# Performance work log

Measured on AMD Instinct MI355X. Metric: run time of the kernel, lower is better.

The kernel has to match this reference:

```python
import jax, jax.numpy as jnp
import numpy as np
from jax import lax

N_PTS = 500000
CH = 64
GRID = 256
BN_EPS = 1e-5
A = -0.75  # torch bicubic coefficient


def setup_inputs() -> dict:
    key = jax.random.key(0)
    ks = jax.random.split(key, 10)
    coordinates = jax.random.uniform(ks[0], (N_PTS, 3), jnp.float32) * 2.0 - 1.0  # points in [-1,1]^3
    noise = jax.random.normal(ks[1], (3, N_PTS, 2), jnp.float32) * 0.01  # per-plane coord jitter (is_training)
    plane_x = jax.random.normal(ks[2], (1, CH, GRID, GRID), jnp.float32) * 0.001
    plane_y = jax.random.normal(ks[3], (1, CH, GRID, GRID), jnp.float32) * 0.001
    plane_z = jax.random.normal(ks[4], (1, CH, GRID, GRID), jnp.float32) * 0.001
    fan_in = CH * 9
    conv_w = jax.random.uniform(ks[5], (CH, CH, 3, 3), jnp.float32, -1.0, 1.0) / np.sqrt(fan_in)
    conv_b = jax.random.uniform(ks[6], (CH,), jnp.float32, -1.0, 1.0) / np.sqrt(fan_in)
    bn_gamma = jnp.ones((CH,), jnp.float32)
    bn_beta = jnp.zeros((CH,), jnp.float32)
    return {"coordinates": coordinates, "noise": noise, "plane_x": plane_x,
            "plane_y": plane_y, "plane_z": plane_z, "conv_w": conv_w,
            "conv_b": conv_b, "bn_gamma": bn_gamma, "bn_beta": bn_beta}


def res_block(p, conv_w, conv_b, gamma, beta):
    # conv3x3 stride2 pad1 -> BN (batch stats, training mode) -> relu, + avgpool3x3 s2 p1 (count_include_pad)
    y = lax.conv_general_dilated(p, conv_w, (2, 2), [(1, 1), (1, 1)],
                                 dimension_numbers=("NCHW", "OIHW", "NCHW"))
    y = y + conv_b[None, :, None, None]
    mu = jnp.mean(y, axis=(0, 2, 3), keepdims=True)
    var = jnp.var(y, axis=(0, 2, 3), keepdims=True)  # biased, as torch BN uses for normalization
    y = (y - mu) * lax.rsqrt(var + BN_EPS) * gamma[None, :, None, None] + beta[None, :, None, None]
    y = jax.nn.relu(y)
    pooled = lax.reduce_window(p, 0.0, lax.add, (1, 1, 3, 3), (1, 1, 2, 2),
                               [(0, 0), (0, 0), (1, 1), (1, 1)]) / 9.0
    return y + pooled


def cubic_weights(t):
    # torch cubic convolution weights, a=-0.75; t in [0,1). returns (4, M)
    t1 = t + 1.0
    w0 = ((A * t1 - 5 * A) * t1 + 8 * A) * t1 - 4 * A
    w1 = ((A + 2) * t - (A + 3)) * t * t + 1.0
    s = 1.0 - t
    w2 = ((A + 2) * s - (A + 3)) * s * s + 1.0
    w3 = 1.0 - w0 - w1 - w2
    return jnp.stack([w0, w1, w2, w3])


def sample_plane_bicubic(plane, grid):
    # plane: (C,H,W); grid: (M,2) with grid[:,0]->W axis, grid[:,1]->H axis (torch grid_sample layout)
    # bicubic, padding_mode='border', align_corners=True
    C, H, W = plane.shape
    gx = jnp.clip((grid[:, 0] + 1.0) * 0.5 * (W - 1), 0.0, W - 1.0)
    gy = jnp.clip((grid[:, 1] + 1.0) * 0.5 * (H - 1), 0.0, H - 1.0)
    x0f = jnp.floor(gx); y0f = jnp.floor(gy)
    tx = gx - x0f; ty = gy - y0f
    x0 = x0f.astype(jnp.int32); y0 = y0f.astype(jnp.int32)
    wx = cubic_weights(tx)  # (4,M)
    wy = cubic_weights(ty)  # (4,M)
    pl = jnp.transpose(plane, (1, 2, 0))  # (H,W,C)
    out = jnp.zeros((grid.shape[0], C), plane.dtype)
    for i in range(4):  # fixed 4x4 bicubic footprint
        yi = jnp.clip(y0 + (i - 1), 0, H - 1)
        for j in range(4):
            xi = jnp.clip(x0 + (j - 1), 0, W - 1)
            out = out + (wy[i] * wx[j])[:, None] * pl[yi, xi]
    return out  # (M,C)


def reference(coordinates, noise, plane_x, plane_y, plane_z, conv_w, conv_b, bn_gamma, bn_beta):
    bound = 1.0
    c = (coordinates + bound) / (2.0 * bound)  # (N,3) in [0,1] (fed to grid_sample as-is, faithful)
    px = res_block(plane_x, conv_w, conv_b, bn_gamma, bn_beta)[0]  # (C,128,128)
    py = res_block(plane_y, conv_w, conv_b, bn_gamma, bn_beta)[0]
    pz = res_block(plane_z, conv_w, conv_b, bn_gamma, bn_beta)[0]
    xy = sample_plane_bicubic(px, c[:, 0:2] + noise[0])
    yz = sample_plane_bicubic(py, c[:, 1:3] + noise[1])
    xz = sample_plane_bicubic(pz, c[:, 0:3:2] + noise[2])
    return xy + yz + xz  # (N,C)
```

## Files before the change

kernel.cpp:

```cpp
#include <hip/hip_runtime.h>
#include <hip/hip_fp16.h>

#define N_POINTS 500000
#define BN_EPS 1e-5f
#define A_COEF -0.75f

typedef __attribute__((ext_vector_type(8))) short short8;
typedef __attribute__((ext_vector_type(4))) float floatx4;
typedef unsigned short ushort_t;
typedef unsigned int uint_t;

#define WS_WBF_OFF    0
#define WS_CONV_OFF   18432
#define WS_SUM_OFF    (WS_CONV_OFF + 3145728)
#define WS_SUMSQ_OFF  (WS_SUM_OFF + 192)
#define WS_SCALE_OFF  (WS_SUMSQ_OFF + 192)
#define WS_SHIFT_OFF  (WS_SCALE_OFF + 192)
#define WS_PLANES_OFF (WS_SHIFT_OFF + 192)
#define WS_INBF_OFF   (WS_PLANES_OFF + 1572864)

__device__ __forceinline__ ushort_t f2bf(float f) {
  uint_t u = __float_as_uint(f);
  uint_t r = (u + 0x7fffu + ((u >> 16) & 1u)) >> 16;
  return (ushort_t)r;
}
__device__ __forceinline__ float bf2f(ushort_t u) {
  return __uint_as_float(((uint_t)u) << 16);
}

__global__ __launch_bounds__(256) void wprep_kernel(const float* __restrict__ w_in,
                                                    float* __restrict__ ws) {
  int i = blockIdx.x * 256 + threadIdx.x;
  if (i < 36864) {
    int ic = i & 63;
    int oc = (i >> 6) & 63;
    int kk = i >> 12;
    ((ushort_t*)(ws + WS_WBF_OFF))[i] = f2bf(w_in[(oc * 64 + ic) * 9 + kk]);
  }
  if (i < 384) ws[WS_SUM_OFF + i] = 0.0f;
}

__global__ __launch_bounds__(256) void transpose_kernel(const float* __restrict__ p0,
                                                        const float* __restrict__ p1,
                                                        const float* __restrict__ p2,
                                                        float* __restrict__ ws) {
  __shared__ float tile[64][65];
  const int xt = blockIdx.x, y = blockIdx.y, pl = blockIdx.z;
  const float* src = (pl == 0) ? p0 : ((pl == 1) ? p1 : p2);
  ushort_t* dst = (ushort_t*)(ws + WS_INBF_OFF) + pl * (256 * 256 * 64);
  const int t = threadIdx.x;
  const int x0 = xt * 64;
  for (int i = t; i < 4096; i += 256) {
    int c = i >> 6, x = i & 63;
    tile[x][c] = src[(c * 256 + y) * 256 + x0 + x];
  }
  __syncthreads();
  uint_t* du = (uint_t*)dst;
  for (int i = t; i < 2048; i += 256) {
    int x = i >> 5, cp = (i & 31) * 2;
    uint_t lo = f2bf(tile[x][cp]);
    uint_t hi = f2bf(tile[x][cp + 1]);
    du[((y * 256 + x0 + x) * 64 + cp) >> 1] = (hi << 16) | lo;
  }
}

__global__ __launch_bounds__(256) void conv_mfma_kernel(const float* __restrict__ ws_r,
                                                        float* __restrict__ ws) {
  const int xh = blockIdx.x, oy = blockIdx.y, pz = blockIdx.z;
  const int t = threadIdx.x;
  const int wv = t >> 6, lane = t & 63;
  const int mn = lane & 15;
  const int kg = lane >> 4;
  const int x0w = xh * 64 + wv * 16;

  const ushort_t* inb = (const ushort_t*)(ws_r + WS_INBF_OFF) + pz * (256 * 256 * 64);
  const ushort_t* wbf = (const ushort_t*)(ws_r + WS_WBF_OFF);

  floatx4 acc[4] = {{0.f,0.f,0.f,0.f},{0.f,0.f,0.f,0.f},{0.f,0.f,0.f,0.f},{0.f,0.f,0.f,0.f}};

  for (int ky = 0; ky < 3; ky++) {
    int y = 2 * oy - 1 + ky;
    if (y < 0) continue;
    const ushort_t* rowp = inb + y * (256 * 64);
    for (int kx = 0; kx < 3; kx++) {
      int xm = 2 * (x0w + mn) - 1 + kx;
      bool vx = xm >= 0;
      int xc = vx ? xm : 0;
      const ushort_t* abase = rowp + xc * 64 + kg * 8;
      const ushort_t* wbase = wbf + ((ky * 3 + kx) * 64 + mn) * 64 + kg * 8;
#pragma unroll
      for (int kc = 0; kc < 2; kc++) {
        union { int4 i4; short8 s8; } au;
        au.i4 = *reinterpret_cast<const int4*>(abase + kc * 32);
        if (!vx) au.i4 = make_int4(0, 0, 0, 0);
#pragma unroll
        for (int nt = 0; nt < 4; nt++) {
          union { int4 i4; short8 s8; } bu;
          bu.i4 = *reinterpret_cast<const int4*>(wbase + nt * 1024 + kc * 32);
          acc[nt] = __builtin_amdgcn_mfma_f32_16x16x32_bf16(au.s8, bu.s8, acc[nt], 0, 0, 0);
        }
      }
    }
  }
  float* cout = ws + WS_CONV_OFF + ((pz * 128 + oy) * 128 + x0w) * 64;
#pragma unroll
  for (int nt = 0; nt < 4; nt++) {
#pragma unroll
    for (int r = 0; r < 4; r++) {
      cout[(kg * 4 + r) * 64 + nt * 16 + mn] = acc[nt][r];
    }
  }
}

__global__ __launch_bounds__(256) void stats_kernel(float* __restrict__ ws) {
  const int b = blockIdx.x;
  const int plane = b >> 6, chunk = b & 63;
  const int t = threadIdx.x;
  const int c = t & 63, g = t >> 6;
  const float* base = ws + WS_CONV_OFF + plane * (16384 * 64);
  float s = 0.0f, s2 = 0.0f;
  const int row0 = chunk * 256 + g * 64;
  for (int i = 0; i < 64; i++) {
    float v = base[(row0 + i) * 64 + c];
    s += v;
    s2 = fmaf(v, v, s2);
  }
  __shared__ float rs[256], rs2[256];
  rs[t] = s; rs2[t] = s2;
  __syncthreads();
  if (t < 64) {
    s = rs[t] + rs[t + 64] + rs[t + 128] + rs[t + 192];
    s2 = rs2[t] + rs2[t + 64] + rs2[t + 128] + rs2[t + 192];
    atomicAdd(&ws[WS_SUM_OFF + plane * 64 + c], s);
    atomicAdd(&ws[WS_SUMSQ_OFF + plane * 64 + c], s2);
  }
}

__global__ void finalize_kernel(const float* __restrict__ gamma,
                                const float* __restrict__ beta,
                                float* __restrict__ ws) {
  int i = threadIdx.x;
  if (i < 192) {
    int c = i & 63;
    float mu = ws[WS_SUM_OFF + i] * (1.0f / 16384.0f);
    float var = ws[WS_SUMSQ_OFF + i] * (1.0f / 16384.0f) - mu * mu;
    var = fmaxf(var, 0.0f);
    float rstd = 1.0f / sqrtf(var + BN_EPS);
    float sc = gamma[c] * rstd;
    ws[WS_SCALE_OFF + i] = sc;
    ws[WS_SHIFT_OFF + i] = beta[c] - mu * sc;
  }
}

__global__ __launch_bounds__(256) void apply_kernel(float* __restrict__ ws,
                                                    __half* __restrict__ planes) {
  int idx = blockIdx.x * 256 + threadIdx.x;
  int g = idx & 7;
  int p = (idx >> 3) & 16383;
  int pl = idx >> 17;
  int oy = p >> 7, ox = p & 127;
  int cb = g * 8;

  const float* conv = ws + WS_CONV_OFF;
  float4 a0 = *reinterpret_cast<const float4*>(conv + (size_t)idx * 8);
  float4 a1 = *reinterpret_cast<const float4*>(conv + (size_t)idx * 8 + 4);

  float sc[8], sh[8];
#pragma unroll
  for (int k = 0; k < 8; k++) {
    sc[k] = ws[WS_SCALE_OFF + pl * 64 + cb + k];
    sh[k] = ws[WS_SHIFT_OFF + pl * 64 + cb + k];
  }

  const ushort_t* inb = (const ushort_t*)(ws + WS_INBF_OFF) + pl * (256 * 256 * 64);
  float ps[8];
#pragma unroll
  for (int k = 0; k < 8; k++) ps[k] = 0.0f;
#pragma unroll
  for (int r = 0; r < 3; r++) {
    int yy = 2 * oy - 1 + r;
    if (yy < 0) continue;
#pragma unroll
    for (int s = 0; s < 3; s++) {
      int xx = 2 * ox - 1 + s;
      if (xx < 0) continue;
      union { int4 i4; ushort_t u[8]; } ub;
      ub.i4 = *reinterpret_cast<const int4*>(inb + (yy * 256 + xx) * 64 + cb);
#pragma unroll
      for (int k = 0; k < 8; k++) ps[k] += bf2f(ub.u[k]);
    }
  }

  float v[8] = {a0.x, a0.y, a0.z, a0.w, a1.x, a1.y, a1.z, a1.w};
  union { int4 i4; __half h[8]; } ob;
#pragma unroll
  for (int k = 0; k < 8; k++) {
    float r = fmaxf(fmaf(v[k], sc[k], sh[k]), 0.0f) + ps[k] * (1.0f / 9.0f);
    ob.h[k] = __float2half(r);
  }
  *reinterpret_cast<int4*>(planes + (size_t)idx * 8) = ob.i4;
}

__device__ __forceinline__ void cubic_w(float t, float w[4]) {
  float t1 = t + 1.0f;
  w[0] = ((A_COEF * t1 - 5.0f * A_COEF) * t1 + 8.0f * A_COEF) * t1 - 4.0f * A_COEF;
  w[1] = ((A_COEF + 2.0f) * t - (A_COEF + 3.0f)) * t * t + 1.0f;
  float s = 1.0f - t;
  w[2] = ((A_COEF + 2.0f) * s - (A_COEF + 3.0f)) * s * s + 1.0f;
  w[3] = 1.0f - w[0] - w[1] - w[2];
}

__global__ __launch_bounds__(256) void sample_kernel(const float* __restrict__ coords,
                                                     const float* __restrict__ noise,
                                                     const __half* __restrict__ planes,
                                                     float* __restrict__ out) {
  const int t = threadIdx.x;
  const int wv = t >> 6, lane = t & 63;
  const int g = lane >> 3, l = lane & 7;
  const int n = blockIdx.x * 32 + wv * 8 + g;

  const float c0 = (coords[n * 3 + 0] + 1.0f) * 0.5f;
  const float c1 = (coords[n * 3 + 1] + 1.0f) * 0.5f;
  const float c2 = (coords[n * 3 + 2] + 1.0f) * 0.5f;

  float acc[8];
#pragma unroll
  for (int e = 0; e < 8; e++) acc[e] = 0.0f;

#pragma unroll
  for (int p = 0; p < 3; p++) {
    float u = (p == 1) ? c1 : c0;
    float v = (p == 0) ? c1 : c2;
    u += noise[(p * N_POINTS + n) * 2 + 0];
    v += noise[(p * N_POINTS + n) * 2 + 1];
    float gx = fminf(fmaxf(fmaf(u, 63.5f, 63.5f), 0.0f), 127.0f);
    float gy = fminf(fmaxf(fmaf(v, 63.5f, 63.5f), 0.0f), 127.0f);
    float x0f = floorf(gx), y0f = floorf(gy);
    float tx = gx - x0f, ty = gy - y0f;
    int ix = (int)x0f, iy = (int)y0f;
    float wx[4], wy[4];
    cubic_w(tx, wx);
    cubic_w(ty, wy);
    const __half* pb = planes + p * (128 * 128 * 64) + l * 8;
#pragma unroll
    for (int i = 0; i < 4; i++) {
      int yc = min(max(iy - 1 + i, 0), 127);
      const __half* rp = pb + yc * (128 * 64);
#pragma unroll
      for (int j = 0; j < 4; j++) {
        int xc = min(max(ix - 1 + j, 0), 127);
        union { int4 i4; __half2 h2[4]; } ub;
        ub.i4 = *reinterpret_cast<const int4*>(rp + xc * 64);
        float w = wy[i] * wx[j];
#pragma unroll
        for (int q = 0; q < 4; q++) {
          float2 f = __half22float2(ub.h2[q]);
          acc[2 * q]     = fmaf(f.x, w, acc[2 * q]);
          acc[2 * q + 1] = fmaf(f.y, w, acc[2 * q + 1]);
        }
      }
    }
  }
  float4* op = reinterpret_cast<float4*>(out + (size_t)n * 64 + l * 8);
  op[0] = make_float4(acc[0], acc[1], acc[2], acc[3]);
  op[1] = make_float4(acc[4], acc[5], acc[6], acc[7]);
}

extern "C" void kernel_launch(void* const* d_in, const int* in_sizes, int n_in,
                              void* d_out, int out_size, void* d_ws, size_t ws_size,
                              hipStream_t stream) {
  const float* coords = (const float*)d_in[0];
  const float* noise  = (const float*)d_in[1];
  const float* px     = (const float*)d_in[2];
  const float* py     = (const float*)d_in[3];
  const float* pz     = (const float*)d_in[4];
  const float* conv_w = (const float*)d_in[5];
  const float* gamma  = (const float*)d_in[7];
  const float* beta   = (const float*)d_in[8];
  float* out = (float*)d_out;
  float* ws = (float*)d_ws;
  __half* planes = (__half*)(ws + WS_PLANES_OFF);

  wprep_kernel<<<144, 256, 0, stream>>>(conv_w, ws);
  transpose_kernel<<<dim3(4, 256, 3), 256, 0, stream>>>(px, py, pz, ws);
  conv_mfma_kernel<<<dim3(2, 128, 3), 256, 0, stream>>>(ws, ws);
  stats_kernel<<<192, 256, 0, stream>>>(ws);
  finalize_kernel<<<1, 256, 0, stream>>>(gamma, beta, ws);
  apply_kernel<<<1536, 256, 0, stream>>>(ws, planes);
  sample_kernel<<<15625, 256, 0, stream>>>(coords, noise, planes, out);
}
```

Baseline: 366.4 us.

## Bin points spatially with a counting sort to localize plane gathers

Adds histogram, scan and scatter kernels that counting-sort the points into a 16x16x16 grid of cells. Each point is written as a packed record holding its three jittered plane coordinates and its original index. The sample kernel then walks the points in cell order, so neighbouring threads gather from nearby plane texels, which should improve L2 reuse of the fp16 planes. The cost is three extra passes over coords and noise, global atomics, and output rows now written in scattered order. The records reuse the bf16 input staging buffer once the conv stage is finished with it.

```diff
diff --git a/kernel.cpp b/kernel.cpp
--- a/kernel.cpp
+++ b/kernel.cpp
@@ -18,6 +18,8 @@
 #define WS_SHIFT_OFF  (WS_SCALE_OFF + 192)
 #define WS_PLANES_OFF (WS_SHIFT_OFF + 192)
 #define WS_INBF_OFF   (WS_PLANES_OFF + 1572864)
+#define WS_REC_OFF    WS_INBF_OFF
+#define WS_BIN_OFF    (WS_INBF_OFF + 6291456)
 
 __device__ __forceinline__ ushort_t f2bf(float f) {
   uint_t u = __float_as_uint(f);
@@ -26,6 +28,12 @@
 }
 __device__ __forceinline__ float bf2f(ushort_t u) {
   return __uint_as_float(((uint_t)u) << 16);
+}
+__device__ __forceinline__ int cell_of(float c0, float c1, float c2) {
+  int q0 = min(15, max(0, (int)(c0 * 16.0f)));
+  int q1 = min(15, max(0, (int)(c1 * 16.0f)));
+  int q2 = min(15, max(0, (int)(c2 * 16.0f)));
+  return (q0 << 8) | (q1 << 4) | q2;
 }
 
 __global__ __launch_bounds__(256) void wprep_kernel(const float* __restrict__ w_in,
@@ -38,6 +46,60 @@
     ((ushort_t*)(ws + WS_WBF_OFF))[i] = f2bf(w_in[(oc * 64 + ic) * 9 + kk]);
   }
   if (i < 384) ws[WS_SUM_OFF + i] = 0.0f;
+  if (i < 8192) ((int*)(ws + WS_BIN_OFF))[i] = 0;
+}
+
+__global__ __launch_bounds__(256) void hist_kernel(const float* __restrict__ coords,
+                                                   float* __restrict__ ws) {
+  int n = blockIdx.x * 256 + threadIdx.x;
+  if (n >= N_POINTS) return;
+  float c0 = (coords[n * 3 + 0] + 1.0f) * 0.5f;
+  float c1 = (coords[n * 3 + 1] + 1.0f) * 0.5f;
+  float c2 = (coords[n * 3 + 2] + 1.0f) * 0.5f;
+  atomicAdd(&((int*)(ws + WS_BIN_OFF))[cell_of(c0, c1, c2)], 1);
+}
+
+__global__ __launch_bounds__(256) void scan_kernel(float* __restrict__ ws) {
+  __shared__ int sums[256];
+  int* hist = (int*)(ws + WS_BIN_OFF);
+  int* offs = hist + 4096;
+  int t = threadIdx.x;
+  int local[16], s = 0;
+#pragma unroll
+  for (int k = 0; k < 16; k++) { local[k] = hist[t * 16 + k]; s += local[k]; }
+  sums[t] = s;
+  __syncthreads();
+  for (int d = 1; d < 256; d <<= 1) {
+    int v = (t >= d) ? sums[t - d] : 0;
+    __syncthreads();
+    sums[t] += v;
+    __syncthreads();
+  }
+  int excl = sums[t] - s;
+#pragma unroll
+  for (int k = 0; k < 16; k++) { offs[t * 16 + k] = excl; excl += local[k]; }
+}
+
+__global__ __launch_bounds__(256) void scatter_kernel(const float* __restrict__ coords,
+                                                      const float* __restrict__ noise,
+                                                      float* __restrict__ ws) {
+  int n = blockIdx.x * 256 + threadIdx.x;
+  if (n >= N_POINTS) return;
+  float c0 = (coords[n * 3 + 0] + 1.0f) * 0.5f;
+  float c1 = (coords[n * 3 + 1] + 1.0f) * 0.5f;
+  float c2 = (coords[n * 3 + 2] + 1.0f) * 0.5f;
+  int cell = cell_of(c0, c1, c2);
+  int* offs = (int*)(ws + WS_BIN_OFF) + 4096;
+  int pos = atomicAdd(&offs[cell], 1);
+  float u0 = c0 + noise[(0 * N_POINTS + n) * 2 + 0];
+  float v0 = c1 + noise[(0 * N_POINTS + n) * 2 + 1];
+  float u1 = c1 + noise[(1 * N_POINTS + n) * 2 + 0];
+  float v1 = c2 + noise[(1 * N_POINTS + n) * 2 + 1];
+  float u2 = c0 + noise[(2 * N_POINTS + n) * 2 + 0];
+  float v2 = c2 + noise[(2 * N_POINTS + n) * 2 + 1];
+  float4* rec = (float4*)(ws + WS_REC_OFF) + pos * 2;
+  rec[0] = make_float4(u0, v0, u1, v1);
+  rec[1] = make_float4(u2, v2, __int_as_float(n), 0.0f);
 }
 
 __global__ __launch_bounds__(256) void transpose_kernel(const float* __restrict__ p0,
@@ -210,53 +272,54 @@
   w[3] = 1.0f - w[0] - w[1] - w[2];
 }
 
-__global__ __launch_bounds__(256) void sample_kernel(const float* __restrict__ coords,
-                                                     const float* __restrict__ noise,
+__global__ __launch_bounds__(256) void sample_kernel(const float* __restrict__ ws,
                                                      const __half* __restrict__ planes,
                                                      float* __restrict__ out) {
   const int t = threadIdx.x;
   const int wv = t >> 6, lane = t & 63;
   const int g = lane >> 3, l = lane & 7;
-  const int n = blockIdx.x * 32 + wv * 8 + g;
-
-  const float c0 = (coords[n * 3 + 0] + 1.0f) * 0.5f;
-  const float c1 = (coords[n * 3 + 1] + 1.0f) * 0.5f;
-  const float c2 = (coords[n * 3 + 2] + 1.0f) * 0.5f;
+  const int idx = blockIdx.x * 32 + wv * 8 + g;
+
+  const float4* rec = (const float4*)(ws + WS_REC_OFF) + (size_t)idx * 2;
+  float4 r0 = rec[0];
+  float4 r1 = rec[1];
+  const int n = __float_as_int(r1.z);
+  float uu[3] = {r0.x, r0.z, r1.x};
+  float vv[3] = {r0.y, r0.w, r1.y};
 
   float acc[8];
 #pragma unroll
   for (int e = 0; e < 8; e++) acc[e] = 0.0f;
 
+  const char* pbase = (const char*)planes + l * 16;
+
 #pragma unroll
   for (int p = 0; p < 3; p++) {
-    float u = (p == 1) ? c1 : c0;
-    float v = (p == 0) ? c1 : c2;
-    u += noise[(p * N_POINTS + n) * 2 + 0];
-    v += noise[(p * N_POINTS + n) * 2 + 1];
-    float gx = fminf(fmaxf(fmaf(u, 63.5f, 63.5f), 0.0f), 127.0f);
-    float gy = fminf(fmaxf(fmaf(v, 63.5f, 63.5f), 0.0f), 127.0f);
+    float gx = fminf(fmaxf(fmaf(uu[p], 63.5f, 63.5f), 0.0f), 127.0f);
+    float gy = fminf(fmaxf(fmaf(vv[p], 63.5f, 63.5f), 0.0f), 127.0f);
     float x0f = floorf(gx), y0f = floorf(gy);
     float tx = gx - x0f, ty = gy - y0f;
     int ix = (int)x0f, iy = (int)y0f;
     float wx[4], wy[4];
     cubic_w(tx, wx);
     cubic_w(ty, wy);
-    const __half* pb = planes + p * (128 * 128 * 64) + l * 8;
+    uint_t yo[4], xo[4];
+#pragma unroll
+    for (int i = 0; i < 4; i++) yo[i] = (uint_t)min(max(iy - 1 + i, 0), 127) * 16384u;
+#pragma unroll
+    for (int j = 0; j < 4; j++) xo[j] = (uint_t)min(max(ix - 1 + j, 0), 127) * 128u;
+    const char* pb = pbase + (size_t)p * 2097152;
 #pragma unroll
     for (int i = 0; i < 4; i++) {
-      int yc = min(max(iy - 1 + i, 0), 127);
-      const __half* rp = pb + yc * (128 * 64);
+      const char* rp = pb + yo[i];
 #pragma unroll
       for (int j = 0; j < 4; j++) {
-        int xc = min(max(ix - 1 + j, 0), 127);
-        union { int4 i4; __half2 h2[4]; } ub;
-        ub.i4 = *reinterpret_cast<const int4*>(rp + xc * 64);
+        union { int4 i4; __half h[8]; } ub;
+        ub.i4 = *reinterpret_cast<const int4*>(rp + xo[j]);
         float w = wy[i] * wx[j];
 #pragma unroll
-        for (int q = 0; q < 4; q++) {
-          float2 f = __half22float2(ub.h2[q]);
-          acc[2 * q]     = fmaf(f.x, w, acc[2 * q]);
-          acc[2 * q + 1] = fmaf(f.y, w, acc[2 * q + 1]);
+        for (int q = 0; q < 8; q++) {
+          acc[q] = fmaf(__half2float(ub.h[q]), w, acc[q]);
         }
       }
     }
@@ -282,10 +345,13 @@
   __half* planes = (__half*)(ws + WS_PLANES_OFF);
 
   wprep_kernel<<<144, 256, 0, stream>>>(conv_w, ws);
+  hist_kernel<<<1954, 256, 0, stream>>>(coords, ws);
+  scan_kernel<<<1, 256, 0, stream>>>(ws);
   transpose_kernel<<<dim3(4, 256, 3), 256, 0, stream>>>(px, py, pz, ws);
   conv_mfma_kernel<<<dim3(2, 128, 3), 256, 0, stream>>>(ws, ws);
   stats_kernel<<<192, 256, 0, stream>>>(ws);
   finalize_kernel<<<1, 256, 0, stream>>>(gamma, beta, ws);
   apply_kernel<<<1536, 256, 0, stream>>>(ws, planes);
-  sample_kernel<<<15625, 256, 0, stream>>>(coords, noise, planes, out);
-}
+  scatter_kernel<<<1954, 256, 0, stream>>>(coords, noise, ws);
+  sample_kernel<<<15625, 256, 0, stream>>>(ws, planes, out);
+}
```

Result: slower. 414.2 us (+13.0%).
